# Optimization experiments

Hardware: AMD Instinct MI355X
Metric: run time of the kernel (lower is better)

The kernel has to match this reference:

```python
import jax, jax.numpy as jnp
import numpy as np

B, T, D = 8, 2048, 1024
E, S = 8, 1            # num_experts, num_slots
FF = 4 * (S * D)       # ffn_mult * (num_slots * hiddens)

def setup_inputs() -> dict:
    key = jax.random.key(0)
    ks = jax.random.split(key, 7)
    sd = S * D
    inp = {
        "X":  jax.random.normal(ks[0], (B, T, D), dtype=jnp.float32),
        # slots gating MLP (single linear D -> E*S)
        "Wg": jax.random.normal(ks[1], (D, E * S), dtype=jnp.float32) / np.sqrt(D),
        "bg": jnp.zeros((E * S,), dtype=jnp.float32),
        # expert FFN (weights SHARED across experts, as in source [FFN(...)]*E)
        "W1": jax.random.normal(ks[2], (sd, FF), dtype=jnp.float32) / np.sqrt(sd),
        "b1": jnp.zeros((FF,), dtype=jnp.float32),
        "W2": jax.random.normal(ks[3], (FF, sd), dtype=jnp.float32) / np.sqrt(FF),
        "b2": jnp.zeros((sd,), dtype=jnp.float32),
    }
    return inp

def reference(X, Wg, bg, W1, b1, W2, b2):
    # logits: (B, T, E*S)
    logits = jnp.einsum('btd,de->bte', X, Wg) + bg
    dispatch_w = jax.nn.softmax(logits, axis=1)   # over tokens T
    combine_w = jax.nn.softmax(logits, axis=2)    # over slots E*S
    # slots = dispatch_w^T @ X : (B, E*S, D) -> (B, E, S*D)
    slots = jnp.einsum('bte,btd->bed', dispatch_w, X).reshape(B, E, S * D)
    # shared-weight FFN applied per expert slot (dropout=0 at eval)
    h = jax.nn.silu(jnp.einsum('bef,fh->beh', slots, W1) + b1)
    y = jnp.einsum('beh,hf->bef', h, W2) + b2     # (B, E, S*D)
    y = y.reshape(B, E * S, D)
    # combine: (B, T, E*S) @ (B, E*S, D)
    return jnp.einsum('bte,bed->btd', combine_w, y)
```

## Files before the change

### kernel.cpp

```cpp
#include <hip/hip_runtime.h>
#include <math.h>

#define B_  8
#define T_  2048
#define D_  1024
#define E_  8
#define FF_ 4096
#define N_  64
#define BT_ (B_*T_)

__global__ __launch_bounds__(256) void k_logits_part(
    const float* __restrict__ X, const float* __restrict__ Wg,
    float* __restrict__ part)
{
    __shared__ float wgT[E_ * 128];
    __shared__ float xt[256 * 36];

    const int tid = threadIdx.x;
    const int bt0 = blockIdx.x * 256;
    const int d0  = blockIdx.y * 128;

    #pragma unroll
    for (int r = 0; r < 4; ++r) {
        int idx = r * 256 + tid;
        wgT[(idx & 7) * 128 + (idx >> 3)] = Wg[(size_t)d0 * E_ + idx];
    }

    float acc[8];
    #pragma unroll
    for (int e = 0; e < 8; ++e) acc[e] = 0.f;

    for (int dt = 0; dt < 4; ++dt) {
        __syncthreads();
        #pragma unroll
        for (int r = 0; r < 8; ++r) {
            int fi = r * 256 + tid;
            int token = fi >> 3, dj = fi & 7;
            const float4 v = *(const float4*)
                &X[(size_t)(bt0 + token) * D_ + d0 + dt * 32 + dj * 4];
            *(float4*)&xt[token * 36 + dj * 4] = v;
        }
        __syncthreads();
        #pragma unroll
        for (int dj = 0; dj < 8; ++dj) {
            const float4 x4 = *(const float4*)&xt[tid * 36 + dj * 4];
            #pragma unroll
            for (int e = 0; e < 8; ++e) {
                const float4 w4 = *(const float4*)&wgT[e * 128 + dt * 32 + dj * 4];
                acc[e] += x4.x * w4.x + x4.y * w4.y + x4.z * w4.z + x4.w * w4.w;
            }
        }
    }

    float* pp = &part[(size_t)blockIdx.y * BT_ * E_ + (size_t)(bt0 + tid) * E_];
    *(float4*)&pp[0] = make_float4(acc[0], acc[1], acc[2], acc[3]);
    *(float4*)&pp[4] = make_float4(acc[4], acc[5], acc[6], acc[7]);
}

__global__ __launch_bounds__(256) void k_logits_merge(
    const float* __restrict__ part, const float* __restrict__ bg,
    float* __restrict__ logits, float* __restrict__ sumexp)
{
    __shared__ float red[8 * 256];
    const int tid = threadIdx.x;
    const int token = blockIdx.x * 256 + tid;
    const int b = blockIdx.x >> 3;

    float a[8];
    #pragma unroll
    for (int e = 0; e < 8; ++e) a[e] = 0.f;
    #pragma unroll
    for (int p = 0; p < 8; ++p) {
        const float* pp = &part[(size_t)p * BT_ * E_ + (size_t)token * E_];
        const float4 v0 = *(const float4*)&pp[0];
        const float4 v1 = *(const float4*)&pp[4];
        a[0] += v0.x; a[1] += v0.y; a[2] += v0.z; a[3] += v0.w;
        a[4] += v1.x; a[5] += v1.y; a[6] += v1.z; a[7] += v1.w;
    }
    #pragma unroll
    for (int e = 0; e < 8; ++e) a[e] += bg[e];

    float* lp = &logits[(size_t)token * E_];
    *(float4*)&lp[0] = make_float4(a[0], a[1], a[2], a[3]);
    *(float4*)&lp[4] = make_float4(a[4], a[5], a[6], a[7]);

    #pragma unroll
    for (int e = 0; e < 8; ++e) red[e * 256 + tid] = expf(a[e]);
    __syncthreads();
    for (int s = 128; s >= 1; s >>= 1) {
        if (tid < s) {
            #pragma unroll
            for (int e = 0; e < 8; ++e)
                red[e * 256 + tid] += red[e * 256 + tid + s];
        }
        __syncthreads();
    }
    if (tid < 8) atomicAdd(&sumexp[b * E_ + tid], red[tid * 256]);
}

__global__ __launch_bounds__(256) void k_slots_part(
    const float* __restrict__ X, const float* __restrict__ logits,
    const float* __restrict__ sumexp, float* __restrict__ part)
{
    __shared__ float wlds[32 * 8];
    const int tid = threadIdx.x;
    const int ts = blockIdx.x, b = blockIdx.y;
    const int t0 = ts * 32;

    {
        int t = tid >> 3, e = tid & 7;
        wlds[tid] = expf(logits[((size_t)b * T_ + t0 + t) * E_ + e])
                    / sumexp[b * E_ + e];
    }
    __syncthreads();

    float4 acc[8];
    #pragma unroll
    for (int e = 0; e < 8; ++e) { acc[e].x = acc[e].y = acc[e].z = acc[e].w = 0.f; }

    const float* xb = &X[((size_t)b * T_ + t0) * D_ + tid * 4];
    #pragma unroll 8
    for (int t = 0; t < 32; ++t) {
        const float4 x4 = *(const float4*)&xb[(size_t)t * D_];
        const float4 wA = *(const float4*)&wlds[t * 8];
        const float4 wB = *(const float4*)&wlds[t * 8 + 4];
        const float w[8] = {wA.x, wA.y, wA.z, wA.w, wB.x, wB.y, wB.z, wB.w};
        #pragma unroll
        for (int e = 0; e < 8; ++e) {
            acc[e].x += x4.x * w[e];
            acc[e].y += x4.y * w[e];
            acc[e].z += x4.z * w[e];
            acc[e].w += x4.w * w[e];
        }
    }
    #pragma unroll
    for (int e = 0; e < 8; ++e) {
        *(float4*)&part[(size_t)ts * (N_ * D_) + (size_t)(b * E_ + e) * D_ + tid * 4] = acc[e];
    }
}

__global__ __launch_bounds__(256) void k_reduce_slots(
    const float* __restrict__ part, float* __restrict__ slots)
{
    const int i = blockIdx.x * 256 + threadIdx.x;
    float s = 0.f;
    #pragma unroll
    for (int p = 0; p < 64; ++p) s += part[(size_t)p * (N_ * D_) + i];
    slots[i] = s;
}

__global__ __launch_bounds__(256) void k_gemm_part(
    const float* __restrict__ A, const float* __restrict__ W,
    float* __restrict__ part, int K, int F)
{
    __shared__ float As[64][64];

    const int tid = threadIdx.x;
    const int rg  = tid >> 5;
    const int cg  = tid & 31;
    const int f0  = blockIdx.x * 128 + cg * 4;
    const int k0  = blockIdx.y * 64;

    #pragma unroll
    for (int i = 0; i < 4; ++i) {
        int idx = i * 256 + tid;
        int row = idx >> 4, kq = idx & 15;
        const float4 v = *(const float4*)&A[(size_t)row * K + k0 + kq * 4];
        *(float4*)&As[row][kq * 4] = v;
    }
    __syncthreads();

    float4 acc[8];
    #pragma unroll
    for (int r = 0; r < 8; ++r) { acc[r].x = acc[r].y = acc[r].z = acc[r].w = 0.f; }

    #pragma unroll 2
    for (int kq = 0; kq < 16; ++kq) {
        float4 w0 = *(const float4*)&W[(size_t)(k0 + kq * 4 + 0) * F + f0];
        float4 w1 = *(const float4*)&W[(size_t)(k0 + kq * 4 + 1) * F + f0];
        float4 w2 = *(const float4*)&W[(size_t)(k0 + kq * 4 + 2) * F + f0];
        float4 w3 = *(const float4*)&W[(size_t)(k0 + kq * 4 + 3) * F + f0];
        #pragma unroll
        for (int r = 0; r < 8; ++r) {
            const float4 a = *(const float4*)&As[rg * 8 + r][kq * 4];
            acc[r].x += a.x * w0.x + a.y * w1.x + a.z * w2.x + a.w * w3.x;
            acc[r].y += a.x * w0.y + a.y * w1.y + a.z * w2.y + a.w * w3.y;
            acc[r].z += a.x * w0.z + a.y * w1.z + a.z * w2.z + a.w * w3.z;
            acc[r].w += a.x * w0.w + a.y * w1.w + a.z * w2.w + a.w * w3.w;
        }
    }

    float* pb = &part[(size_t)blockIdx.y * N_ * F];
    #pragma unroll
    for (int r = 0; r < 8; ++r)
        *(float4*)&pb[(size_t)(rg * 8 + r) * F + f0] = acc[r];
}

__global__ __launch_bounds__(256) void k_reduce_silu(
    const float* __restrict__ part, const float* __restrict__ b1,
    float* __restrict__ h)
{
    const int i = blockIdx.x * 256 + threadIdx.x;
    float s = 0.f;
    #pragma unroll
    for (int p = 0; p < 16; ++p) s += part[(size_t)p * (N_ * FF_) + i];
    s += b1[i & (FF_ - 1)];
    h[i] = s / (1.f + expf(-s));
}

__global__ __launch_bounds__(256) void k_reduce_bias(
    const float* __restrict__ part, const float* __restrict__ b2,
    float* __restrict__ y)
{
    const int i = blockIdx.x * 256 + threadIdx.x;
    float s = 0.f;
    #pragma unroll
    for (int p = 0; p < 64; ++p) s += part[(size_t)p * (N_ * D_) + i];
    y[i] = s + b2[i & (D_ - 1)];
}

__global__ __launch_bounds__(256) void k_combine(
    const float* __restrict__ logits, const float* __restrict__ y,
    float* __restrict__ out)
{
    __shared__ float wlds[64 * 8];
    const int tid = threadIdx.x;
    const int dc = blockIdx.x, tc = blockIdx.y, b = blockIdx.z;
    const int t0 = tc * 64;

    if (tid < 64) {
        const float* lp = &logits[((size_t)b * T_ + t0 + tid) * E_];
        float ex[8]; float s = 0.f;
        #pragma unroll
        for (int i = 0; i < 8; ++i) { ex[i] = expf(lp[i]); s += ex[i]; }
        const float invs = 1.f / s;
        #pragma unroll
        for (int i = 0; i < 8; ++i) wlds[tid * 8 + i] = ex[i] * invs;
    }
    __syncthreads();

    const int d = dc * 256 + tid;
    float yv[8];
    #pragma unroll
    for (int e = 0; e < 8; ++e) yv[e] = y[(size_t)(b * E_ + e) * D_ + d];

    for (int t = 0; t < 64; ++t) {
        const float4 wA = *(const float4*)&wlds[t * 8];
        const float4 wB = *(const float4*)&wlds[t * 8 + 4];
        const float acc = wA.x * yv[0] + wA.y * yv[1] + wA.z * yv[2] + wA.w * yv[3]
                        + wB.x * yv[4] + wB.y * yv[5] + wB.z * yv[6] + wB.w * yv[7];
        out[((size_t)b * T_ + t0 + t) * D_ + d] = acc;
    }
}

extern "C" void kernel_launch(void* const* d_in, const int* in_sizes, int n_in,
                              void* d_out, int out_size, void* d_ws, size_t ws_size,
                              hipStream_t stream)
{
    const float* X  = (const float*)d_in[0];
    const float* Wg = (const float*)d_in[1];
    const float* bg = (const float*)d_in[2];
    const float* W1 = (const float*)d_in[3];
    const float* b1 = (const float*)d_in[4];
    const float* W2 = (const float*)d_in[5];
    const float* b2 = (const float*)d_in[6];
    float* out = (float*)d_out;

    float* wsf    = (float*)d_ws;
    float* logits = wsf;
    float* sumexp = logits + BT_ * E_;
    float* slots  = sumexp + 64;
    float* h      = slots + N_ * D_;
    float* y      = h + N_ * FF_;

    float* part = out;

    hipMemsetAsync(sumexp, 0, 64 * sizeof(float), stream);

    hipLaunchKernelGGL(k_logits_part,  dim3(BT_ / 256, 8), dim3(256), 0, stream,
                       X, Wg, part);
    hipLaunchKernelGGL(k_logits_merge, dim3(BT_ / 256),    dim3(256), 0, stream,
                       part, bg, logits, sumexp);
    hipLaunchKernelGGL(k_slots_part,   dim3(64, 8),        dim3(256), 0, stream,
                       X, logits, sumexp, part);
    hipLaunchKernelGGL(k_reduce_slots, dim3(256),          dim3(256), 0, stream,
                       part, slots);
    hipLaunchKernelGGL(k_gemm_part,    dim3(FF_ / 128, 1024 / 64), dim3(256), 0, stream,
                       slots, W1, part, 1024, FF_);
    hipLaunchKernelGGL(k_reduce_silu,  dim3(N_ * FF_ / 256), dim3(256), 0, stream,
                       part, b1, h);
    hipLaunchKernelGGL(k_gemm_part,    dim3(D_ / 128, FF_ / 64), dim3(256), 0, stream,
                       h, W2, part, FF_, D_);
    hipLaunchKernelGGL(k_reduce_bias,  dim3(N_ * D_ / 256), dim3(256), 0, stream,
                       part, b2, y);
    hipLaunchKernelGGL(k_combine,      dim3(4, 32, 8), dim3(256), 0, stream,
                       logits, y, out);
}
```

Before: 260.4 us.

## Fuse all stages into one persistent megakernel with software grid barriers

Replaces nine separate kernel launches plus reductions with a single persistent kernel of 512 blocks. The stages are separated by atomic-counter grid barriers. It also restructures the softmax-over-tokens normalization: per-chunk exp sums are written out and the division is folded into the slot reduction, replacing the atomicAdd into sumexp. The goal is to remove launch gaps and tail effects. The barriers rely on all 512 blocks being co-resident (launch_bounds 256,2), and the spin-wait has a guard that can silently break, so correctness depends on occupancy.

```diff
diff --git a/kernel.cpp b/kernel.cpp
--- a/kernel.cpp
+++ b/kernel.cpp
@@ -8,248 +8,259 @@
 #define FF_ 4096
 #define N_  64
 #define BT_ (B_*T_)
-
-__global__ __launch_bounds__(256) void k_logits_part(
-    const float* __restrict__ X, const float* __restrict__ Wg,
-    float* __restrict__ part)
-{
-    __shared__ float wgT[E_ * 128];
-    __shared__ float xt[256 * 36];
-
+#define NBLK 512
+
+#define LPART_F  0u
+#define SPART_F  1048576u
+#define G1PART_F 3145728u
+#define G2PART_F 7340032u
+
+__device__ __forceinline__ void gsync(int* bar, int target)
+{
+    __syncthreads();
+    if (threadIdx.x == 0) {
+        __threadfence();
+        atomicAdd(bar, 1);
+        int guard = 0;
+        while (atomicAdd(bar, 0) < target) {
+            __builtin_amdgcn_s_sleep(32);
+            if (++guard > (1 << 24)) break;
+        }
+        __threadfence();
+    }
+    __syncthreads();
+}
+
+template<int K, int F>
+__device__ __forceinline__ void gemm_phase(
+    const float* __restrict__ A, const float* __restrict__ W,
+    float* __restrict__ part, float* As, int fc, int kc)
+{
     const int tid = threadIdx.x;
-    const int bt0 = blockIdx.x * 256;
-    const int d0  = blockIdx.y * 128;
-
-    #pragma unroll
-    for (int r = 0; r < 4; ++r) {
-        int idx = r * 256 + tid;
-        wgT[(idx & 7) * 128 + (idx >> 3)] = Wg[(size_t)d0 * E_ + idx];
-    }
-
-    float acc[8];
-    #pragma unroll
-    for (int e = 0; e < 8; ++e) acc[e] = 0.f;
-
-    for (int dt = 0; dt < 4; ++dt) {
-        __syncthreads();
-        #pragma unroll
-        for (int r = 0; r < 8; ++r) {
-            int fi = r * 256 + tid;
-            int token = fi >> 3, dj = fi & 7;
-            const float4 v = *(const float4*)
-                &X[(size_t)(bt0 + token) * D_ + d0 + dt * 32 + dj * 4];
-            *(float4*)&xt[token * 36 + dj * 4] = v;
-        }
-        __syncthreads();
-        #pragma unroll
-        for (int dj = 0; dj < 8; ++dj) {
-            const float4 x4 = *(const float4*)&xt[tid * 36 + dj * 4];
-            #pragma unroll
-            for (int e = 0; e < 8; ++e) {
-                const float4 w4 = *(const float4*)&wgT[e * 128 + dt * 32 + dj * 4];
-                acc[e] += x4.x * w4.x + x4.y * w4.y + x4.z * w4.z + x4.w * w4.w;
-            }
-        }
-    }
-
-    float* pp = &part[(size_t)blockIdx.y * BT_ * E_ + (size_t)(bt0 + tid) * E_];
-    *(float4*)&pp[0] = make_float4(acc[0], acc[1], acc[2], acc[3]);
-    *(float4*)&pp[4] = make_float4(acc[4], acc[5], acc[6], acc[7]);
-}
-
-__global__ __launch_bounds__(256) void k_logits_merge(
-    const float* __restrict__ part, const float* __restrict__ bg,
-    float* __restrict__ logits, float* __restrict__ sumexp)
-{
-    __shared__ float red[8 * 256];
-    const int tid = threadIdx.x;
-    const int token = blockIdx.x * 256 + tid;
-    const int b = blockIdx.x >> 3;
-
-    float a[8];
-    #pragma unroll
-    for (int e = 0; e < 8; ++e) a[e] = 0.f;
-    #pragma unroll
-    for (int p = 0; p < 8; ++p) {
-        const float* pp = &part[(size_t)p * BT_ * E_ + (size_t)token * E_];
-        const float4 v0 = *(const float4*)&pp[0];
-        const float4 v1 = *(const float4*)&pp[4];
-        a[0] += v0.x; a[1] += v0.y; a[2] += v0.z; a[3] += v0.w;
-        a[4] += v1.x; a[5] += v1.y; a[6] += v1.z; a[7] += v1.w;
-    }
-    #pragma unroll
-    for (int e = 0; e < 8; ++e) a[e] += bg[e];
-
-    float* lp = &logits[(size_t)token * E_];
-    *(float4*)&lp[0] = make_float4(a[0], a[1], a[2], a[3]);
-    *(float4*)&lp[4] = make_float4(a[4], a[5], a[6], a[7]);
-
-    #pragma unroll
-    for (int e = 0; e < 8; ++e) red[e * 256 + tid] = expf(a[e]);
-    __syncthreads();
-    for (int s = 128; s >= 1; s >>= 1) {
-        if (tid < s) {
-            #pragma unroll
-            for (int e = 0; e < 8; ++e)
-                red[e * 256 + tid] += red[e * 256 + tid + s];
-        }
-        __syncthreads();
-    }
-    if (tid < 8) atomicAdd(&sumexp[b * E_ + tid], red[tid * 256]);
-}
-
-__global__ __launch_bounds__(256) void k_slots_part(
-    const float* __restrict__ X, const float* __restrict__ logits,
-    const float* __restrict__ sumexp, float* __restrict__ part)
-{
-    __shared__ float wlds[32 * 8];
-    const int tid = threadIdx.x;
-    const int ts = blockIdx.x, b = blockIdx.y;
-    const int t0 = ts * 32;
-
-    {
-        int t = tid >> 3, e = tid & 7;
-        wlds[tid] = expf(logits[((size_t)b * T_ + t0 + t) * E_ + e])
-                    / sumexp[b * E_ + e];
-    }
-    __syncthreads();
-
-    float4 acc[8];
-    #pragma unroll
-    for (int e = 0; e < 8; ++e) { acc[e].x = acc[e].y = acc[e].z = acc[e].w = 0.f; }
-
-    const float* xb = &X[((size_t)b * T_ + t0) * D_ + tid * 4];
-    #pragma unroll 8
-    for (int t = 0; t < 32; ++t) {
-        const float4 x4 = *(const float4*)&xb[(size_t)t * D_];
-        const float4 wA = *(const float4*)&wlds[t * 8];
-        const float4 wB = *(const float4*)&wlds[t * 8 + 4];
-        const float w[8] = {wA.x, wA.y, wA.z, wA.w, wB.x, wB.y, wB.z, wB.w};
-        #pragma unroll
-        for (int e = 0; e < 8; ++e) {
-            acc[e].x += x4.x * w[e];
-            acc[e].y += x4.y * w[e];
-            acc[e].z += x4.z * w[e];
-            acc[e].w += x4.w * w[e];
-        }
-    }
-    #pragma unroll
-    for (int e = 0; e < 8; ++e) {
-        *(float4*)&part[(size_t)ts * (N_ * D_) + (size_t)(b * E_ + e) * D_ + tid * 4] = acc[e];
-    }
-}
-
-__global__ __launch_bounds__(256) void k_reduce_slots(
-    const float* __restrict__ part, float* __restrict__ slots)
-{
-    const int i = blockIdx.x * 256 + threadIdx.x;
-    float s = 0.f;
-    #pragma unroll
-    for (int p = 0; p < 64; ++p) s += part[(size_t)p * (N_ * D_) + i];
-    slots[i] = s;
-}
-
-__global__ __launch_bounds__(256) void k_gemm_part(
-    const float* __restrict__ A, const float* __restrict__ W,
-    float* __restrict__ part, int K, int F)
-{
-    __shared__ float As[64][64];
-
-    const int tid = threadIdx.x;
-    const int rg  = tid >> 5;
-    const int cg  = tid & 31;
-    const int f0  = blockIdx.x * 128 + cg * 4;
-    const int k0  = blockIdx.y * 64;
+    const int rg = tid >> 5, cg = tid & 31;
+    const int f0 = fc * 128 + cg * 4;
+    const int k0 = kc * 64;
 
     #pragma unroll
     for (int i = 0; i < 4; ++i) {
         int idx = i * 256 + tid;
         int row = idx >> 4, kq = idx & 15;
-        const float4 v = *(const float4*)&A[(size_t)row * K + k0 + kq * 4];
-        *(float4*)&As[row][kq * 4] = v;
+        *(float4*)&As[row * 64 + kq * 4] =
+            *(const float4*)&A[(size_t)row * K + k0 + kq * 4];
     }
     __syncthreads();
 
     float4 acc[8];
     #pragma unroll
-    for (int r = 0; r < 8; ++r) { acc[r].x = acc[r].y = acc[r].z = acc[r].w = 0.f; }
+    for (int r = 0; r < 8; ++r) acc[r] = make_float4(0.f, 0.f, 0.f, 0.f);
 
     #pragma unroll 2
     for (int kq = 0; kq < 16; ++kq) {
-        float4 w0 = *(const float4*)&W[(size_t)(k0 + kq * 4 + 0) * F + f0];
-        float4 w1 = *(const float4*)&W[(size_t)(k0 + kq * 4 + 1) * F + f0];
-        float4 w2 = *(const float4*)&W[(size_t)(k0 + kq * 4 + 2) * F + f0];
-        float4 w3 = *(const float4*)&W[(size_t)(k0 + kq * 4 + 3) * F + f0];
+        const float* wr = &W[(size_t)(k0 + kq * 4) * F + f0];
+        const float4 w0 = *(const float4*)&wr[0];
+        const float4 w1 = *(const float4*)&wr[(size_t)F];
+        const float4 w2 = *(const float4*)&wr[(size_t)2 * F];
+        const float4 w3 = *(const float4*)&wr[(size_t)3 * F];
         #pragma unroll
         for (int r = 0; r < 8; ++r) {
-            const float4 a = *(const float4*)&As[rg * 8 + r][kq * 4];
-            acc[r].x += a.x * w0.x + a.y * w1.x + a.z * w2.x + a.w * w3.x;
-            acc[r].y += a.x * w0.y + a.y * w1.y + a.z * w2.y + a.w * w3.y;
-            acc[r].z += a.x * w0.z + a.y * w1.z + a.z * w2.z + a.w * w3.z;
-            acc[r].w += a.x * w0.w + a.y * w1.w + a.z * w2.w + a.w * w3.w;
-        }
-    }
-
-    float* pb = &part[(size_t)blockIdx.y * N_ * F];
+            const float4 a = *(const float4*)&As[(rg * 8 + r) * 64 + kq * 4];
+            acc[r].x += a.x*w0.x + a.y*w1.x + a.z*w2.x + a.w*w3.x;
+            acc[r].y += a.x*w0.y + a.y*w1.y + a.z*w2.y + a.w*w3.y;
+            acc[r].z += a.x*w0.z + a.y*w1.z + a.z*w2.z + a.w*w3.z;
+            acc[r].w += a.x*w0.w + a.y*w1.w + a.z*w2.w + a.w*w3.w;
+        }
+    }
+    float* pb = &part[(size_t)kc * N_ * F];
     #pragma unroll
     for (int r = 0; r < 8; ++r)
         *(float4*)&pb[(size_t)(rg * 8 + r) * F + f0] = acc[r];
 }
 
-__global__ __launch_bounds__(256) void k_reduce_silu(
-    const float* __restrict__ part, const float* __restrict__ b1,
-    float* __restrict__ h)
-{
-    const int i = blockIdx.x * 256 + threadIdx.x;
-    float s = 0.f;
-    #pragma unroll
-    for (int p = 0; p < 16; ++p) s += part[(size_t)p * (N_ * FF_) + i];
-    s += b1[i & (FF_ - 1)];
-    h[i] = s / (1.f + expf(-s));
-}
-
-__global__ __launch_bounds__(256) void k_reduce_bias(
-    const float* __restrict__ part, const float* __restrict__ b2,
-    float* __restrict__ y)
-{
-    const int i = blockIdx.x * 256 + threadIdx.x;
-    float s = 0.f;
-    #pragma unroll
-    for (int p = 0; p < 64; ++p) s += part[(size_t)p * (N_ * D_) + i];
-    y[i] = s + b2[i & (D_ - 1)];
-}
-
-__global__ __launch_bounds__(256) void k_combine(
-    const float* __restrict__ logits, const float* __restrict__ y,
-    float* __restrict__ out)
-{
-    __shared__ float wlds[64 * 8];
+__global__ __launch_bounds__(256, 2) void k_mega(
+    const float* __restrict__ X, const float* __restrict__ Wg,
+    const float* __restrict__ bg, const float* __restrict__ W1,
+    const float* __restrict__ b1, const float* __restrict__ W2,
+    const float* __restrict__ b2, float* __restrict__ outbuf,
+    float* __restrict__ logits, float* __restrict__ sexp,
+    float* __restrict__ slots, float* __restrict__ h,
+    float* __restrict__ y, int* bar)
+{
+    __shared__ float lds[9216];
     const int tid = threadIdx.x;
-    const int dc = blockIdx.x, tc = blockIdx.y, b = blockIdx.z;
-    const int t0 = tc * 64;
-
-    if (tid < 64) {
-        const float* lp = &logits[((size_t)b * T_ + t0 + tid) * E_];
-        float ex[8]; float s = 0.f;
-        #pragma unroll
-        for (int i = 0; i < 8; ++i) { ex[i] = expf(lp[i]); s += ex[i]; }
-        const float invs = 1.f / s;
-        #pragma unroll
-        for (int i = 0; i < 8; ++i) wlds[tid * 8 + i] = ex[i] * invs;
-    }
-    __syncthreads();
-
-    const int d = dc * 256 + tid;
-    float yv[8];
-    #pragma unroll
-    for (int e = 0; e < 8; ++e) yv[e] = y[(size_t)(b * E_ + e) * D_ + d];
-
-    for (int t = 0; t < 64; ++t) {
-        const float4 wA = *(const float4*)&wlds[t * 8];
-        const float4 wB = *(const float4*)&wlds[t * 8 + 4];
-        const float acc = wA.x * yv[0] + wA.y * yv[1] + wA.z * yv[2] + wA.w * yv[3]
-                        + wB.x * yv[4] + wB.y * yv[5] + wB.z * yv[6] + wB.w * yv[7];
-        out[((size_t)b * T_ + t0 + t) * D_ + d] = acc;
+    const int vb  = blockIdx.x;
+
+    {
+        const int bt0 = (vb & 63) * 256;
+        const int d0  = (vb >> 6) * 128;
+        float acc[8];
+        #pragma unroll
+        for (int e = 0; e < 8; ++e) acc[e] = 0.f;
+
+        for (int dt = 0; dt < 4; ++dt) {
+            if (dt) __syncthreads();
+            #pragma unroll
+            for (int r = 0; r < 8; ++r) {
+                int fi = r * 256 + tid;
+                int token = fi >> 3, dj = fi & 7;
+                const float4 v = *(const float4*)
+                    &X[(size_t)(bt0 + token) * D_ + d0 + dt * 32 + dj * 4];
+                *(float4*)&lds[token * 36 + dj * 4] = v;
+            }
+            __syncthreads();
+            #pragma unroll
+            for (int dj = 0; dj < 8; ++dj) {
+                const float4 x4 = *(const float4*)&lds[tid * 36 + dj * 4];
+                const int db = d0 + dt * 32 + dj * 4;
+                const float xv[4] = {x4.x, x4.y, x4.z, x4.w};
+                #pragma unroll
+                for (int rr = 0; rr < 4; ++rr) {
+                    const float4 wlo = *(const float4*)&Wg[(size_t)(db + rr) * 8];
+                    const float4 whi = *(const float4*)&Wg[(size_t)(db + rr) * 8 + 4];
+                    acc[0] += xv[rr]*wlo.x; acc[1] += xv[rr]*wlo.y;
+                    acc[2] += xv[rr]*wlo.z; acc[3] += xv[rr]*wlo.w;
+                    acc[4] += xv[rr]*whi.x; acc[5] += xv[rr]*whi.y;
+                    acc[6] += xv[rr]*whi.z; acc[7] += xv[rr]*whi.w;
+                }
+            }
+        }
+        float* pp = &outbuf[LPART_F + (size_t)(vb >> 6) * BT_ * E_
+                            + (size_t)(bt0 + tid) * E_];
+        *(float4*)&pp[0] = make_float4(acc[0], acc[1], acc[2], acc[3]);
+        *(float4*)&pp[4] = make_float4(acc[4], acc[5], acc[6], acc[7]);
+    }
+    gsync(bar, NBLK);
+
+    if (vb < 256) {
+        const int ts = vb & 31, b = vb >> 5;
+        const int t0 = ts * 64;
+        float* wlds = lds;
+
+        #pragma unroll
+        for (int r = 0; r < 2; ++r) {
+            int idx = r * 256 + tid;
+            int t = idx >> 3, e = idx & 7;
+            float a = bg[e];
+            #pragma unroll
+            for (int dc = 0; dc < 8; ++dc)
+                a += outbuf[LPART_F + (size_t)dc * BT_ * E_
+                            + ((size_t)b * T_ + t0 + t) * E_ + e];
+            logits[((size_t)b * T_ + t0 + t) * E_ + e] = a;
+            wlds[idx] = expf(a);
+        }
+        __syncthreads();
+        if (tid < 8) {
+            float s = 0.f;
+            for (int t = 0; t < 64; ++t) s += wlds[t * 8 + tid];
+            sexp[(b * 32 + ts) * 8 + tid] = s;
+        }
+
+        float4 acc[8];
+        #pragma unroll
+        for (int e = 0; e < 8; ++e) acc[e] = make_float4(0.f, 0.f, 0.f, 0.f);
+
+        const float* xb = &X[((size_t)b * T_ + t0) * D_ + tid * 4];
+        #pragma unroll 8
+        for (int t = 0; t < 64; ++t) {
+            const float4 x4 = *(const float4*)&xb[(size_t)t * D_];
+            const float4 wA = *(const float4*)&wlds[t * 8];
+            const float4 wB = *(const float4*)&wlds[t * 8 + 4];
+            const float w[8] = {wA.x, wA.y, wA.z, wA.w, wB.x, wB.y, wB.z, wB.w};
+            #pragma unroll
+            for (int e = 0; e < 8; ++e) {
+                acc[e].x += x4.x * w[e];
+                acc[e].y += x4.y * w[e];
+                acc[e].z += x4.z * w[e];
+                acc[e].w += x4.w * w[e];
+            }
+        }
+        #pragma unroll
+        for (int e = 0; e < 8; ++e)
+            *(float4*)&outbuf[SPART_F + (size_t)ts * (N_ * D_)
+                              + (size_t)(b * E_ + e) * D_ + tid * 4] = acc[e];
+    }
+    gsync(bar, 2 * NBLK);
+
+    {
+        const int gid = vb * 256 + tid;
+        if (gid < 65536) {
+            const int row = gid >> 10;
+            const int b = row >> 3, e = row & 7;
+            float se = 0.f;
+            #pragma unroll
+            for (int t = 0; t < 32; ++t) se += sexp[(b * 32 + t) * 8 + e];
+            float s = 0.f;
+            #pragma unroll
+            for (int p = 0; p < 32; ++p)
+                s += outbuf[SPART_F + (size_t)p * (N_ * D_) + gid];
+            slots[gid] = s / se;
+        }
+    }
+    gsync(bar, 3 * NBLK);
+
+    gemm_phase<1024, 4096>(slots, W1, &outbuf[G1PART_F], lds, vb >> 4, vb & 15);
+    gsync(bar, 4 * NBLK);
+
+    {
+        #pragma unroll
+        for (int s = 0; s < 2; ++s) {
+            const int i = s * 131072 + vb * 256 + tid;
+            float v = b1[i & (FF_ - 1)];
+            #pragma unroll
+            for (int p = 0; p < 16; ++p)
+                v += outbuf[G1PART_F + (size_t)p * (N_ * FF_) + i];
+            h[i] = v / (1.f + expf(-v));
+        }
+    }
+    gsync(bar, 5 * NBLK);
+
+    gemm_phase<4096, 1024>(h, W2, &outbuf[G2PART_F], lds, vb >> 6, vb & 63);
+    gsync(bar, 6 * NBLK);
+
+    {
+        const int gid = vb * 256 + tid;
+        if (gid < 65536) {
+            float v = b2[gid & (D_ - 1)];
+            #pragma unroll
+            for (int p = 0; p < 64; ++p)
+                v += outbuf[G2PART_F + (size_t)p * (N_ * D_) + gid];
+            y[gid] = v;
+        }
+    }
+    gsync(bar, 7 * NBLK);
+
+    {
+        float* wlds = lds;
+        #pragma unroll
+        for (int s = 0; s < 2; ++s) {
+            const int cb = vb * 2 + s;
+            const int dc = cb & 3, tc = (cb >> 2) & 31, b = cb >> 7;
+            const int t0 = tc * 64;
+
+            __syncthreads();
+            if (tid < 64) {
+                const float* lp = &logits[((size_t)b * T_ + t0 + tid) * E_];
+                float ex[8]; float sm = 0.f;
+                #pragma unroll
+                for (int i = 0; i < 8; ++i) { ex[i] = expf(lp[i]); sm += ex[i]; }
+                const float invs = 1.f / sm;
+                #pragma unroll
+                for (int i = 0; i < 8; ++i) wlds[tid * 8 + i] = ex[i] * invs;
+            }
+            __syncthreads();
+
+            const int d = dc * 256 + tid;
+            float yv[8];
+            #pragma unroll
+            for (int e = 0; e < 8; ++e) yv[e] = y[(size_t)(b * E_ + e) * D_ + d];
+
+            for (int t = 0; t < 64; ++t) {
+                const float4 wA = *(const float4*)&wlds[t * 8];
+                const float4 wB = *(const float4*)&wlds[t * 8 + 4];
+                const float acc = wA.x*yv[0] + wA.y*yv[1] + wA.z*yv[2] + wA.w*yv[3]
+                                + wB.x*yv[4] + wB.y*yv[5] + wB.z*yv[6] + wB.w*yv[7];
+                outbuf[((size_t)b * T_ + t0 + t) * D_ + d] = acc;
+            }
+        }
     }
 }
 
@@ -267,32 +278,15 @@
     float* out = (float*)d_out;
 
     float* wsf    = (float*)d_ws;
-    float* logits = wsf;
-    float* sumexp = logits + BT_ * E_;
-    float* slots  = sumexp + 64;
+    int*   bar    = (int*)d_ws;
+    float* logits = wsf + 64;
+    float* sexp   = logits + BT_ * E_;
+    float* slots  = sexp + 2048;
     float* h      = slots + N_ * D_;
     float* y      = h + N_ * FF_;
 
-    float* part = out;
-
-    hipMemsetAsync(sumexp, 0, 64 * sizeof(float), stream);
-
-    hipLaunchKernelGGL(k_logits_part,  dim3(BT_ / 256, 8), dim3(256), 0, stream,
-                       X, Wg, part);
-    hipLaunchKernelGGL(k_logits_merge, dim3(BT_ / 256),    dim3(256), 0, stream,
-                       part, bg, logits, sumexp);
-    hipLaunchKernelGGL(k_slots_part,   dim3(64, 8),        dim3(256), 0, stream,
-                       X, logits, sumexp, part);
-    hipLaunchKernelGGL(k_reduce_slots, dim3(256),          dim3(256), 0, stream,
-                       part, slots);
-    hipLaunchKernelGGL(k_gemm_part,    dim3(FF_ / 128, 1024 / 64), dim3(256), 0, stream,
-                       slots, W1, part, 1024, FF_);
-    hipLaunchKernelGGL(k_reduce_silu,  dim3(N_ * FF_ / 256), dim3(256), 0, stream,
-                       part, b1, h);
-    hipLaunchKernelGGL(k_gemm_part,    dim3(D_ / 128, FF_ / 64), dim3(256), 0, stream,
-                       h, W2, part, FF_, D_);
-    hipLaunchKernelGGL(k_reduce_bias,  dim3(N_ * D_ / 256), dim3(256), 0, stream,
-                       part, b2, y);
-    hipLaunchKernelGGL(k_combine,      dim3(4, 32, 8), dim3(256), 0, stream,
-                       logits, y, out);
-}
+    hipMemsetAsync(d_ws, 0, 256, stream);
+    hipLaunchKernelGGL(k_mega, dim3(NBLK), dim3(256), 0, stream,
+                       X, Wg, bg, W1, b1, W2, b2, out,
+                       logits, sexp, slots, h, y, bar);
+}
```

Result: slower. 616.5 us (+136.7%).
